# Kernel tuning notes

Hardware: AMD Instinct MI355X
Metric: run time of the kernel (lower is better)

Reference implementation:

```python
import jax, jax.numpy as jnp
import numpy as np

N_HEADS = 4
LEAKY_SLOPE = 0.2


def setup_inputs() -> dict:
    key = jax.random.key(0)
    k1, k2, k3 = jax.random.split(key, 3)
    b, c, h, w = 8, 64, 128, 128
    z = jax.random.normal(k1, (b, c, h, w), dtype=jnp.float32)
    # torch.nn.Linear weights are (out_features, in_features); scale ~1/sqrt(fan_in)
    W_Q = jax.random.normal(k2, (c, c), dtype=jnp.float32) * 0.125
    W_K = jax.random.normal(k3, (c, c), dtype=jnp.float32) * 0.125
    return {"z": z, "W_Q": W_Q, "W_K": W_K}


def _axial_branch(z_perm_flat, z_raw_flat, W_Q, W_K, n_batch, seq, d_k, scale):
    # z_perm_flat: (n_batch, seq, c)  -- rearranged input fed to W_Q
    # z_raw_flat : (n_batch, seq, c)  -- raw memory-order reshape fed to W_K
    Q = jnp.matmul(z_perm_flat, W_Q.T).reshape(N_HEADS * n_batch, d_k, seq)
    V = jnp.matmul(z_raw_flat, W_K.T).reshape(N_HEADS * n_batch, d_k, seq)
    # QK-less scores: Q^T Q / sqrt(d_k)  -> (N, seq, seq)
    scores = jnp.einsum('nds,ndt->nst', Q, Q) * scale
    attn = jax.nn.softmax(scores, axis=-1)
    # right-multiply attention onto V, then LeakyReLU
    ctx = jnp.einsum('nds,nst->ndt', V, attn)
    return jax.nn.leaky_relu(ctx, negative_slope=LEAKY_SLOPE)


def reference(z, W_Q, W_K):
    b, c, h, w = z.shape
    d_k = c // N_HEADS
    scale = 1.0 / np.sqrt(d_k).astype(np.float32)

    # Branch 1 (attention over w): a = rearrange 'b c h w -> (b h) w c'
    a = jnp.transpose(z, (0, 2, 3, 1)).reshape(b * h, w, c)
    v1_in = z.reshape(b * h, w, c)  # raw reshape, as in the torch code
    context1 = _axial_branch(a, v1_in, W_Q, W_K, b * h, w, d_k, scale)

    # Branch 2 (attention over h): m = rearrange 'b c h w -> (b w) h c'
    m = jnp.transpose(z, (0, 3, 2, 1)).reshape(b * w, h, c)
    v2_in = z.reshape(b * w, h, c)  # raw reshape, as in the torch code
    context2 = _axial_branch(m, v2_in, W_Q, W_K, b * w, h, d_k, scale)

    context = context1 + context2  # requires h == w
    return context.reshape(b, c, h, w)
```

## Files before the change

kernel.cpp:

```cpp
#include <hip/hip_runtime.h>


typedef __attribute__((ext_vector_type(8))) short bh8;
typedef __attribute__((ext_vector_type(4))) float f32x4;
typedef unsigned short u16;
typedef unsigned int u32;

#define MFMA16(a,b,c) __builtin_amdgcn_mfma_f32_16x16x32_bf16(a,b,c,0,0,0)

#define AIMG_ST 72
#define QP_ST   40
#define VH_ST   136
#define PT_ST   64

#define OFF_AH   0
#define OFF_AL   4608
#define OFF_VIN  9216
#define OFF_PT   0
#define OFF_QP   16384
#define OFF_VH   26624
#define LDS_TOT  30976

__device__ __forceinline__ u32 cvtpk_rn(float f0, float f1) {
#if __has_builtin(__builtin_amdgcn_cvt_pk_bf16_f32)
    auto h = __builtin_amdgcn_cvt_pk_bf16_f32(f0, f1);
    u32 r; __builtin_memcpy(&r, &h, sizeof(r)); return r;
#else
    return ((__float_as_uint(f0) + 0x8000u) >> 16) |
           ((__float_as_uint(f1) + 0x8000u) & 0xFFFF0000u);
#endif
}
__device__ __forceinline__ float fexp2(float x) {
#if __has_builtin(__builtin_amdgcn_exp2f)
    return __builtin_amdgcn_exp2f(x);
#else
    return exp2f(x);
#endif
}
__device__ __forceinline__ float frcp(float x) {
#if __has_builtin(__builtin_amdgcn_rcpf)
    return __builtin_amdgcn_rcpf(x);
#else
    return 1.0f / x;
#endif
}
__device__ __forceinline__ void splitpk(float f0, float f1, u32& hp, u32& lp) {
    u32 u0 = __float_as_uint(f0), u1 = __float_as_uint(f1);
    hp = __builtin_amdgcn_perm(u1, u0, 0x07060302u);
    float r0 = f0 - __uint_as_float(u0 & 0xFFFF0000u);
    float r1 = f1 - __uint_as_float(u1 & 0xFFFF0000u);
    lp = cvtpk_rn(r0, r1);
}
__device__ __forceinline__ void split3(float f, u16& h, u16& l) {
    u32 u = __float_as_uint(f);
    u32 hf = u & 0xFFFF0000u;
    float r = f - __uint_as_float(hf);
    h = (u16)(hf >> 16);
    l = (u16)((__float_as_uint(r) + 0x8000u) >> 16);
}
__device__ __forceinline__ u16 rnbf(float f) {
    return (u16)((__float_as_uint(f) + 0x8000u) >> 16);
}
__device__ __forceinline__ float lrelu(float x) { return x > 0.f ? x : 0.2f * x; }

__global__ void split_w_kernel(const float* __restrict__ Wq,
                               const float* __restrict__ Wk,
                               u16* __restrict__ ws)
{
    const int i = blockIdx.x * 256 + threadIdx.x;
    const int j = i & 4095;
    const float scale = (i < 4096) ? 0.6005612043932249f : 1.0f;
    const float f = ((i < 4096) ? Wq[j] : Wk[j]) * scale;
    const int base = (i < 4096) ? 0 : 8192;
    u16 h, l; split3(f, h, l);
    ws[base + j] = h;
    ws[base + 4096 + j] = l;
}

#define WOFF(n, ks) (((n)*16 + lid)*64 + (ks)*32 + quad*8)

__device__ __forceinline__ void gemm_q(const u16* Ah, const u16* Al,
                                       const u16* wsu,
                                       u16* qp, int miQ, int niA, int lid, int quad)
{
    const bh8 h0a = *(const bh8*)(wsu +        WOFF(niA+0,0));
    const bh8 h0b = *(const bh8*)(wsu +        WOFF(niA+0,1));
    const bh8 h1a = *(const bh8*)(wsu +        WOFF(niA+1,0));
    const bh8 h1b = *(const bh8*)(wsu +        WOFF(niA+1,1));
    const bh8 l0a = *(const bh8*)(wsu + 4096 + WOFF(niA+0,0));
    const bh8 l0b = *(const bh8*)(wsu + 4096 + WOFF(niA+0,1));
    const bh8 l1a = *(const bh8*)(wsu + 4096 + WOFF(niA+1,0));
    const bh8 l1b = *(const bh8*)(wsu + 4096 + WOFF(niA+1,1));
    const int offA = (miQ*16 + lid)*AIMG_ST + quad*8;
    bh8 ah0 = *(const bh8*)(Ah + offA);
    bh8 ah1 = *(const bh8*)(Ah + offA + 32);
    bh8 al0 = *(const bh8*)(Al + offA);
    bh8 al1 = *(const bh8*)(Al + offA + 32);
    f32x4 acc0 = {0.f,0.f,0.f,0.f}, acc1 = {0.f,0.f,0.f,0.f};
    acc0 = MFMA16(ah0, h0a, acc0); acc0 = MFMA16(ah0, l0a, acc0); acc0 = MFMA16(al0, h0a, acc0);
    acc0 = MFMA16(ah1, h0b, acc0); acc0 = MFMA16(ah1, l0b, acc0); acc0 = MFMA16(al1, h0b, acc0);
    acc1 = MFMA16(ah0, h1a, acc1); acc1 = MFMA16(ah0, l1a, acc1); acc1 = MFMA16(al0, h1a, acc1);
    acc1 = MFMA16(ah1, h1b, acc1); acc1 = MFMA16(ah1, l1b, acc1); acc1 = MFMA16(al1, h1b, acc1);
    const int d0 = miQ*8 + quad*2;
    const int rA = (niA+0)*16 + lid;
    const int rB = (niA+1)*16 + lid;
    u32 h, l;
    splitpk(acc0[0], acc0[2], h, l);
    *(u32*)(qp + rA*QP_ST + d0)       = h;  *(u32*)(qp + rA*QP_ST + 16 + d0)       = l;
    splitpk(acc0[1], acc0[3], h, l);
    *(u32*)(qp + (64+rA)*QP_ST + d0)  = h;  *(u32*)(qp + (64+rA)*QP_ST + 16 + d0)  = l;
    splitpk(acc1[0], acc1[2], h, l);
    *(u32*)(qp + rB*QP_ST + d0)       = h;  *(u32*)(qp + rB*QP_ST + 16 + d0)       = l;
    splitpk(acc1[1], acc1[3], h, l);
    *(u32*)(qp + (64+rB)*QP_ST + d0)  = h;  *(u32*)(qp + (64+rB)*QP_ST + 16 + d0)  = l;
}

__device__ __forceinline__ void gemm_v(const u16* Vin, const u16* wsu,
                                       u16* vh, int miQ, int niA, int lid, int quad)
{
    const bh8 h0a = *(const bh8*)(wsu + 8192 + WOFF(niA+0,0));
    const bh8 h0b = *(const bh8*)(wsu + 8192 + WOFF(niA+0,1));
    const bh8 h1a = *(const bh8*)(wsu + 8192 + WOFF(niA+1,0));
    const bh8 h1b = *(const bh8*)(wsu + 8192 + WOFF(niA+1,1));
    const int offA = (miQ*16 + lid)*AIMG_ST + quad*8;
    bh8 ah0 = *(const bh8*)(Vin + offA);
    bh8 ah1 = *(const bh8*)(Vin + offA + 32);
    f32x4 acc0 = {0.f,0.f,0.f,0.f}, acc1 = {0.f,0.f,0.f,0.f};
    acc0 = MFMA16(ah0, h0a, acc0); acc0 = MFMA16(ah1, h0b, acc0);
    acc1 = MFMA16(ah0, h1a, acc1); acc1 = MFMA16(ah1, h1b, acc1);
    #pragma unroll
    for (int r = 0; r < 4; ++r) {
        const int l = miQ*16 + quad*4 + r;
        const int d = l >> 1;
        const int sbase = (l & 1) << 6;
        vh[d*VH_ST + sbase + (niA + 0)*16 + lid] = rnbf(acc0[r]);
        vh[d*VH_ST + sbase + (niA + 1)*16 + lid] = rnbf(acc1[r]);
    }
}

__device__ __forceinline__ void gram_pt(const u16* Qp, u16* PT, int h,
                                        int w, int lid, int quad)
{
    const u16* arow = Qp + (h*64 + 16*w + lid)*QP_ST;
    const bh8 a_hl = *(const bh8*)(arow + quad*8);
    const bh8 a_lh = *(const bh8*)(arow + ((quad+2)&3)*8);
    f32x4 g[8];
    #pragma unroll
    for (int ti = 0; ti < 8; ++ti) {
        const bh8 b = *(const bh8*)(Qp + (ti*16 + lid)*QP_ST + quad*8);
        f32x4 acc = {0.f,0.f,0.f,0.f};
        acc = MFMA16(a_hl, b, acc);
        acc = MFMA16(a_lh, b, acc);
        g[ti] = acc;
    }
    float inv[4];
    #pragma unroll
    for (int r = 0; r < 4; ++r) {
        float s = 0.f;
        #pragma unroll
        for (int ti = 0; ti < 8; ++ti) {
            const float p = fexp2(g[ti][r]);
            g[ti][r] = p; s += p;
        }
        s += __shfl_xor(s, 1); s += __shfl_xor(s, 2);
        s += __shfl_xor(s, 4); s += __shfl_xor(s, 8);
        inv[r] = frcp(s);
    }
    const int X  = 2*(lid & 7);
    const int uc = ((4*w + quad) ^ X) << 2;
    #pragma unroll
    for (int ti = 0; ti < 8; ++ti) {
        uint2 dv;
        dv.x = cvtpk_rn(g[ti][0]*inv[0], g[ti][1]*inv[1]);
        dv.y = cvtpk_rn(g[ti][2]*inv[2], g[ti][3]*inv[3]);
        *(uint2*)(PT + (ti*16 + lid)*PT_ST + uc) = dv;
    }
}

__device__ __forceinline__ void pv_ctx(const u16* PT, const u16* Vh, int h,
                                       f32x4& c0, f32x4& c1, int w, int lid, int quad)
{
    const int X = 2*(lid & 7);
    const bh8 vb0 = *(const bh8*)(Vh + lid*VH_ST + h*64 +      quad*8);
    const bh8 vb1 = *(const bh8*)(Vh + lid*VH_ST + h*64 + 32 + quad*8);
    #pragma unroll
    for (int tj2 = 0; tj2 < 2; ++tj2) {
        const int tj = 2*w + tj2;
        const bh8 pa0 = *(const bh8*)(PT + (tj*16 + lid)*PT_ST + (((    2*quad) ^ X) << 2));
        const bh8 pa1 = *(const bh8*)(PT + (tj*16 + lid)*PT_ST + (((8 + 2*quad) ^ X) << 2));
        f32x4 acc = tj2 ? c1 : c0;
        acc = MFMA16(pa0, vb0, acc);
        acc = MFMA16(pa1, vb1, acc);
        if (tj2) c1 = acc; else c0 = acc;
    }
}

__global__ __launch_bounds__(256, 4)
void axial_attn_mfma(const float* __restrict__ z, const u16* __restrict__ wsu,
                     float* __restrict__ out)
{
    __shared__ __align__(16) unsigned char lds[LDS_TOT];
    u16* const ptAh = (u16*)(lds + OFF_AH);
    u16* const ptAl = (u16*)(lds + OFF_AL);
    u16* const ptPT = (u16*)(lds + OFF_PT);
    u16* const ptVI = (u16*)(lds + OFF_VIN);
    u16* const ptQP = (u16*)(lds + OFF_QP);
    u16* const ptVH = (u16*)(lds + OFF_VH);

    const int tid = threadIdx.x;
    const int w = tid >> 6, lane = tid & 63, quad = lane >> 4, lid = lane & 15;

    const int blk = blockIdx.x;
    const int j   = blk >> 3;
    const int xi  = ((blk & 7) << 4) | (j & 15);
    const int q   = (j >> 4) & 3;
    const int bi  = j >> 6;
    const int N   = (((bi << 7) | xi) << 2) | q;
    const size_t zbase = (size_t)bi << 20;

    const int c8 = tid >> 5, l5 = tid & 31;
    const int vl0 = tid >> 4, vc0 = (tid & 15) << 2;
    const int miQ = w >> 1, niA = (w & 1) * 2;

    float a1r[8], a2r[8];
    float4 v4[2];
    {
        const float* s1 = z + zbase + ((size_t)xi << 7) + (q << 5) + l5;
        const float* s2 = z + zbase + (((size_t)(q*32 + l5)) << 7) + xi;
        #pragma unroll
        for (int k = 0; k < 8; ++k)
            a1r[k] = s1[(size_t)(c8*8 + k) << 14];
        const float4* sv = (const float4*)(z + ((size_t)N << 11));
        v4[0] = sv[tid]; v4[1] = sv[tid + 256];
        #pragma unroll
        for (int k = 0; k < 8; ++k)
            a2r[k] = s2[(size_t)(c8*8 + k) << 14];
    }

    {
        u32 hp[4], lp[4];
        #pragma unroll
        for (int k = 0; k < 4; ++k) splitpk(a1r[2*k], a1r[2*k+1], hp[k], lp[k]);
        *(uint4*)(ptAh + l5*AIMG_ST + c8*8) = make_uint4(hp[0], hp[1], hp[2], hp[3]);
        *(uint4*)(ptAl + l5*AIMG_ST + c8*8) = make_uint4(lp[0], lp[1], lp[2], lp[3]);
    }
    #pragma unroll
    for (int k = 0; k < 2; ++k) {
        const float4 vv = v4[k];
        uint2 dv;
        dv.x = cvtpk_rn(vv.x, vv.y);
        dv.y = cvtpk_rn(vv.z, vv.w);
        *(uint2*)(ptVI + (vl0 + 16*k)*AIMG_ST + vc0) = dv;
    }
    __syncthreads();

    gemm_q(ptAh, ptAl, wsu, ptQP, miQ, niA, lid, quad);
    gemm_v(ptVI, wsu, ptVH, miQ, niA, lid, quad);
    __syncthreads();

    f32x4 c10 = {0.f,0.f,0.f,0.f}, c11 = {0.f,0.f,0.f,0.f};
    gram_pt(ptQP, ptPT, 0, w, lid, quad);
    __syncthreads();
    pv_ctx(ptPT, ptVH, 0, c10, c11, w, lid, quad);
    __syncthreads();
    gram_pt(ptQP, ptPT, 1, w, lid, quad);
    __syncthreads();
    pv_ctx(ptPT, ptVH, 1, c10, c11, w, lid, quad);
    __syncthreads();

    {
        u32 hp[4], lp[4];
        #pragma unroll
        for (int k = 0; k < 4; ++k) splitpk(a2r[2*k], a2r[2*k+1], hp[k], lp[k]);
        *(uint4*)(ptAh + l5*AIMG_ST + c8*8) = make_uint4(hp[0], hp[1], hp[2], hp[3]);
        *(uint4*)(ptAl + l5*AIMG_ST + c8*8) = make_uint4(lp[0], lp[1], lp[2], lp[3]);
    }
    __syncthreads();

    gemm_q(ptAh, ptAl, wsu, ptQP, miQ, niA, lid, quad);
    __syncthreads();

    f32x4 c20 = {0.f,0.f,0.f,0.f}, c21 = {0.f,0.f,0.f,0.f};
    gram_pt(ptQP, ptPT, 0, w, lid, quad);
    __syncthreads();
    pv_ctx(ptPT, ptVH, 0, c20, c21, w, lid, quad);
    __syncthreads();
    gram_pt(ptQP, ptPT, 1, w, lid, quad);
    __syncthreads();
    pv_ctx(ptPT, ptVH, 1, c20, c21, w, lid, quad);

    float* ob = out + ((size_t)N << 11) + lid*128;
    #pragma unroll
    for (int tj2 = 0; tj2 < 2; ++tj2) {
        f32x4 a = tj2 ? c11 : c10;
        f32x4 b = tj2 ? c21 : c20;
        float4 ov;
        ov.x = lrelu(a[0]) + lrelu(b[0]);
        ov.y = lrelu(a[1]) + lrelu(b[1]);
        ov.z = lrelu(a[2]) + lrelu(b[2]);
        ov.w = lrelu(a[3]) + lrelu(b[3]);
        *(float4*)(ob + (2*w + tj2)*16 + quad*4) = ov;
    }
}

extern "C" void kernel_launch(void* const* d_in, const int* in_sizes, int n_in,
                              void* d_out, int out_size, void* d_ws, size_t ws_size,
                              hipStream_t stream) {
    const float* z  = (const float*)d_in[0];
    const float* Wq = (const float*)d_in[1];
    const float* Wk = (const float*)d_in[2];
    float* out = (float*)d_out;
    u16* ws = (u16*)d_ws;
    hipLaunchKernelGGL(split_w_kernel, dim3(32), dim3(256), 0, stream, Wq, Wk, ws);
    hipLaunchKernelGGL(axial_attn_mfma, dim3(4096), dim3(256), 0, stream, z, ws, out);
}
```

Measured before the change: 153.8 us.

## Keep softmax probabilities in registers and fold normalization into V scaling

Gram tiles are recomputed so each wave owns columns of the score matrix. The exponentiated scores stay in registers as packed bf16 MFMA operands instead of being written to a PT buffer in LDS. Row sums are accumulated into a shared array with LDS atomics, and the 1/sum normalization is applied to V before the PV product. This removes the PT LDS round trip and several barriers per branch and shrinks LDS, at the cost of more registers (pk arrays) and an extra scale pass plus atomics.

```diff
diff --git a/kernel.cpp b/kernel.cpp
--- a/kernel.cpp
+++ b/kernel.cpp
@@ -11,15 +11,14 @@
 #define AIMG_ST 72
 #define QP_ST   40
 #define VH_ST   136
-#define PT_ST   64
+#define VS_ST   136
 
 #define OFF_AH   0
 #define OFF_AL   4608
 #define OFF_VIN  9216
-#define OFF_PT   0
-#define OFF_QP   16384
-#define OFF_VH   26624
-#define LDS_TOT  30976
+#define OFF_QP   13824
+#define OFF_VH   24064
+#define LDS_BLOB 28416
 
 __device__ __forceinline__ u32 cvtpk_rn(float f0, float f1) {
 #if __has_builtin(__builtin_amdgcn_cvt_pk_bf16_f32)
@@ -61,7 +60,14 @@
 __device__ __forceinline__ u16 rnbf(float f) {
     return (u16)((__float_as_uint(f) + 0x8000u) >> 16);
 }
+__device__ __forceinline__ float b2f(short v) {
+    return __uint_as_float(((u32)(u16)v) << 16);
+}
 __device__ __forceinline__ float lrelu(float x) { return x > 0.f ? x : 0.2f * x; }
+__device__ __forceinline__ bh8 mk8(u32 a, u32 b, u32 c, u32 d) {
+    union { bh8 v; u32 u[4]; } x;
+    x.u[0] = a; x.u[1] = b; x.u[2] = c; x.u[3] = d; return x.v;
+}
 
 __global__ void split_w_kernel(const float* __restrict__ Wq,
                                const float* __restrict__ Wk,
@@ -138,60 +144,65 @@
     }
 }
 
-__device__ __forceinline__ void gram_pt(const u16* Qp, u16* PT, int h,
+__device__ __forceinline__ void gram_branch(const u16* Qp, float* TOT,
+                                            u32 pk[8][2][2], int w, int lid, int quad)
+{
+    const bh8 b0 = *(const bh8*)(Qp + (32*w +      lid)*QP_ST + quad*8);
+    const bh8 b1 = *(const bh8*)(Qp + (32*w + 16 + lid)*QP_ST + quad*8);
+    #pragma unroll
+    for (int mt = 0; mt < 8; ++mt) {
+        const u16* arow = Qp + (16*mt + lid)*QP_ST;
+        const bh8 a_hl = *(const bh8*)(arow + quad*8);
+        const bh8 a_lh = *(const bh8*)(arow + ((quad+2)&3)*8);
+        f32x4 g0 = {0.f,0.f,0.f,0.f}, g1 = {0.f,0.f,0.f,0.f};
+        g0 = MFMA16(a_hl, b0, g0); g0 = MFMA16(a_lh, b0, g0);
+        g1 = MFMA16(a_hl, b1, g1); g1 = MFMA16(a_lh, b1, g1);
+        const float p00 = fexp2(g0[0]), p01 = fexp2(g0[1]);
+        const float p02 = fexp2(g0[2]), p03 = fexp2(g0[3]);
+        const float p10 = fexp2(g1[0]), p11 = fexp2(g1[1]);
+        const float p12 = fexp2(g1[2]), p13 = fexp2(g1[3]);
+        pk[mt][0][0] = cvtpk_rn(p00, p01); pk[mt][0][1] = cvtpk_rn(p02, p03);
+        pk[mt][1][0] = cvtpk_rn(p10, p11); pk[mt][1][1] = cvtpk_rn(p12, p13);
+        float s0 = p00 + p10, s1 = p01 + p11, s2 = p02 + p12, s3 = p03 + p13;
+        s0 += __shfl_xor(s0,1); s0 += __shfl_xor(s0,2); s0 += __shfl_xor(s0,4); s0 += __shfl_xor(s0,8);
+        s1 += __shfl_xor(s1,1); s1 += __shfl_xor(s1,2); s1 += __shfl_xor(s1,4); s1 += __shfl_xor(s1,8);
+        s2 += __shfl_xor(s2,1); s2 += __shfl_xor(s2,2); s2 += __shfl_xor(s2,4); s2 += __shfl_xor(s2,8);
+        s3 += __shfl_xor(s3,1); s3 += __shfl_xor(s3,2); s3 += __shfl_xor(s3,4); s3 += __shfl_xor(s3,8);
+        if (lid == mt) {
+            atomicAdd(&TOT[16*mt + 4*quad + 0], s0);
+            atomicAdd(&TOT[16*mt + 4*quad + 1], s1);
+            atomicAdd(&TOT[16*mt + 4*quad + 2], s2);
+            atomicAdd(&TOT[16*mt + 4*quad + 3], s3);
+        }
+    }
+}
+
+__device__ __forceinline__ void scale_v(const u16* Vh, u16* VS, const float* TOT,
                                         int w, int lid, int quad)
 {
-    const u16* arow = Qp + (h*64 + 16*w + lid)*QP_ST;
-    const bh8 a_hl = *(const bh8*)(arow + quad*8);
-    const bh8 a_lh = *(const bh8*)(arow + ((quad+2)&3)*8);
-    f32x4 g[8];
-    #pragma unroll
-    for (int ti = 0; ti < 8; ++ti) {
-        const bh8 b = *(const bh8*)(Qp + (ti*16 + lid)*QP_ST + quad*8);
-        f32x4 acc = {0.f,0.f,0.f,0.f};
-        acc = MFMA16(a_hl, b, acc);
-        acc = MFMA16(a_lh, b, acc);
-        g[ti] = acc;
-    }
-    float inv[4];
-    #pragma unroll
-    for (int r = 0; r < 4; ++r) {
-        float s = 0.f;
-        #pragma unroll
-        for (int ti = 0; ti < 8; ++ti) {
-            const float p = fexp2(g[ti][r]);
-            g[ti][r] = p; s += p;
-        }
-        s += __shfl_xor(s, 1); s += __shfl_xor(s, 2);
-        s += __shfl_xor(s, 4); s += __shfl_xor(s, 8);
-        inv[r] = frcp(s);
-    }
-    const int X  = 2*(lid & 7);
-    const int uc = ((4*w + quad) ^ X) << 2;
-    #pragma unroll
-    for (int ti = 0; ti < 8; ++ti) {
-        uint2 dv;
-        dv.x = cvtpk_rn(g[ti][0]*inv[0], g[ti][1]*inv[1]);
-        dv.y = cvtpk_rn(g[ti][2]*inv[2], g[ti][3]*inv[3]);
-        *(uint2*)(PT + (ti*16 + lid)*PT_ST + uc) = dv;
-    }
-}
-
-__device__ __forceinline__ void pv_ctx(const u16* PT, const u16* Vh, int h,
-                                       f32x4& c0, f32x4& c1, int w, int lid, int quad)
-{
-    const int X = 2*(lid & 7);
-    const bh8 vb0 = *(const bh8*)(Vh + lid*VH_ST + h*64 +      quad*8);
-    const bh8 vb1 = *(const bh8*)(Vh + lid*VH_ST + h*64 + 32 + quad*8);
-    #pragma unroll
-    for (int tj2 = 0; tj2 < 2; ++tj2) {
-        const int tj = 2*w + tj2;
-        const bh8 pa0 = *(const bh8*)(PT + (tj*16 + lid)*PT_ST + (((    2*quad) ^ X) << 2));
-        const bh8 pa1 = *(const bh8*)(PT + (tj*16 + lid)*PT_ST + (((8 + 2*quad) ^ X) << 2));
-        f32x4 acc = tj2 ? c1 : c0;
-        acc = MFMA16(pa0, vb0, acc);
-        acc = MFMA16(pa1, vb1, acc);
-        if (tj2) c1 = acc; else c0 = acc;
+    const int s0 = 32*w + 8*quad;
+    const float4 t0 = *(const float4*)(TOT + s0);
+    const float4 t1 = *(const float4*)(TOT + s0 + 4);
+    const bh8 vr = *(const bh8*)(Vh + lid*VH_ST + s0);
+    const u32 w0 = cvtpk_rn(b2f(vr[0])*frcp(t0.x), b2f(vr[1])*frcp(t0.y));
+    const u32 w1 = cvtpk_rn(b2f(vr[2])*frcp(t0.z), b2f(vr[3])*frcp(t0.w));
+    const u32 w2 = cvtpk_rn(b2f(vr[4])*frcp(t1.x), b2f(vr[5])*frcp(t1.y));
+    const u32 w3 = cvtpk_rn(b2f(vr[6])*frcp(t1.z), b2f(vr[7])*frcp(t1.w));
+    const int tb = ((8*w + 2*quad) & 15)*8 + (w >> 1)*4;
+    *(uint2*)(VS + lid*VS_ST + tb)     = make_uint2(w0, w1);
+    *(uint2*)(VS + lid*VS_ST + tb + 8) = make_uint2(w2, w3);
+}
+
+__device__ __forceinline__ void pv_branch(const u16* VS, const u32 pk[8][2][2],
+                                          f32x4& c0, f32x4& c1, int lid, int quad)
+{
+    #pragma unroll
+    for (int ks = 0; ks < 4; ++ks) {
+        const bh8 vb = *(const bh8*)(VS + lid*VS_ST + 32*ks + 8*quad);
+        const bh8 a0 = mk8(pk[ks][0][0], pk[ks][0][1], pk[ks+4][0][0], pk[ks+4][0][1]);
+        const bh8 a1 = mk8(pk[ks][1][0], pk[ks][1][1], pk[ks+4][1][0], pk[ks+4][1][1]);
+        c0 = MFMA16(a0, vb, c0);
+        c1 = MFMA16(a1, vb, c1);
     }
 }
 
@@ -199,11 +210,12 @@
 void axial_attn_mfma(const float* __restrict__ z, const u16* __restrict__ wsu,
                      float* __restrict__ out)
 {
-    __shared__ __align__(16) unsigned char lds[LDS_TOT];
+    __shared__ __align__(16) unsigned char lds[LDS_BLOB];
+    __shared__ __align__(16) float sTOT[2][128];
     u16* const ptAh = (u16*)(lds + OFF_AH);
     u16* const ptAl = (u16*)(lds + OFF_AL);
-    u16* const ptPT = (u16*)(lds + OFF_PT);
     u16* const ptVI = (u16*)(lds + OFF_VIN);
+    u16* const ptVS = (u16*)(lds + OFF_VIN);
     u16* const ptQP = (u16*)(lds + OFF_QP);
     u16* const ptVH = (u16*)(lds + OFF_VH);
 
@@ -237,6 +249,7 @@
             a2r[k] = s2[(size_t)(c8*8 + k) << 14];
     }
 
+    ((float*)sTOT)[tid] = 0.f;
     {
         u32 hp[4], lp[4];
         #pragma unroll
@@ -258,14 +271,10 @@
     gemm_v(ptVI, wsu, ptVH, miQ, niA, lid, quad);
     __syncthreads();
 
-    f32x4 c10 = {0.f,0.f,0.f,0.f}, c11 = {0.f,0.f,0.f,0.f};
-    gram_pt(ptQP, ptPT, 0, w, lid, quad);
-    __syncthreads();
-    pv_ctx(ptPT, ptVH, 0, c10, c11, w, lid, quad);
-    __syncthreads();
-    gram_pt(ptQP, ptPT, 1, w, lid, quad);
-    __syncthreads();
-    pv_ctx(ptPT, ptVH, 1, c10, c11, w, lid, quad);
+    u32 pk1[8][2][2];
+    gram_branch(ptQP, &sTOT[0][0], pk1, w, lid, quad);
+    __syncthreads();
+    scale_v(ptVH, ptVS, &sTOT[0][0], w, lid, quad);
     __syncthreads();
 
     {
@@ -275,19 +284,20 @@
         *(uint4*)(ptAh + l5*AIMG_ST + c8*8) = make_uint4(hp[0], hp[1], hp[2], hp[3]);
         *(uint4*)(ptAl + l5*AIMG_ST + c8*8) = make_uint4(lp[0], lp[1], lp[2], lp[3]);
     }
+    f32x4 c10 = {0.f,0.f,0.f,0.f}, c11 = {0.f,0.f,0.f,0.f};
+    pv_branch(ptVS, pk1, c10, c11, lid, quad);
     __syncthreads();
 
     gemm_q(ptAh, ptAl, wsu, ptQP, miQ, niA, lid, quad);
     __syncthreads();
 
+    u32 pk2[8][2][2];
+    gram_branch(ptQP, &sTOT[1][0], pk2, w, lid, quad);
+    __syncthreads();
+    scale_v(ptVH, ptVS, &sTOT[1][0], w, lid, quad);
+    __syncthreads();
     f32x4 c20 = {0.f,0.f,0.f,0.f}, c21 = {0.f,0.f,0.f,0.f};
-    gram_pt(ptQP, ptPT, 0, w, lid, quad);
-    __syncthreads();
-    pv_ctx(ptPT, ptVH, 0, c20, c21, w, lid, quad);
-    __syncthreads();
-    gram_pt(ptQP, ptPT, 1, w, lid, quad);
-    __syncthreads();
-    pv_ctx(ptPT, ptVH, 1, c20, c21, w, lid, quad);
+    pv_branch(ptVS, pk2, c20, c21, lid, quad);
 
     float* ob = out + ((size_t)N << 11) + lid*128;
     #pragma unroll
```

Measured after the change: 177.0 us. 15.1% more time.
